# Kernel optimization log

Measured on AMD Instinct MI355X. Metric: run time of the kernel, lower is better.

Reference implementation:

```python
import jax, jax.numpy as jnp
import numpy as np

NUM_EXPERTS = 64
TOP_K = 8
NUM_TOKENS = 8192
HIDDEN = 1024
INTER = 512


def setup_inputs() -> dict:
    key = jax.random.key(0)
    k1, k2, k3, k4 = jax.random.split(key, 4)
    # 0.02 scale keeps activations in a sane range (randn weights with fan-in 1024)
    return {
        "hidden_states": jax.random.normal(k1, (NUM_TOKENS, HIDDEN), jnp.float32),
        "router_weight": jax.random.normal(k2, (HIDDEN, NUM_EXPERTS), jnp.float32) * 0.02,
        "merged_gate_up_proj": jax.random.normal(k3, (NUM_EXPERTS, HIDDEN, 2 * INTER), jnp.float32) * 0.02,
        "merged_down_proj": jax.random.normal(k4, (NUM_EXPERTS, INTER, HIDDEN), jnp.float32) * 0.02,
    }


def reference(hidden_states, router_weight, merged_gate_up_proj, merged_down_proj):
    T, H = hidden_states.shape
    E = router_weight.shape[1]

    # ---- Router: softmax over experts, top-k, renormalize top-k weights ----
    logits = hidden_states @ router_weight                       # [T, E]
    probs = jax.nn.softmax(logits, axis=-1)
    routing_weights, routing_indices = jax.lax.top_k(probs, TOP_K)  # [T, k]
    routing_weights = routing_weights / routing_weights.sum(-1, keepdims=True)

    # ---- Permute (haojun_permute_topk): replicate tokens topk times, stable-sort by expert ----
    flat_indices = routing_indices.reshape(-1)                   # [T*k]
    sort_order = jnp.argsort(flat_indices)                       # stable sort
    flat_states = jnp.repeat(hidden_states, TOP_K, axis=0)       # [T*k, H]
    permuted = flat_states[sort_order]                           # tokens grouped by expert
    group_sizes = jnp.bincount(flat_indices, length=E).astype(jnp.int32)  # tokens per expert

    # ---- Grouped MLP (grouped_gemm.gmm equivalent): y_i = x_i @ W[expert(i)] ----
    merged = jax.lax.ragged_dot(permuted, merged_gate_up_proj, group_sizes)  # [T*k, 2*I]
    gate, up = jnp.split(merged, 2, axis=-1)
    h = jax.nn.silu(gate) * up                                   # SiLU-gated (hidden_act='silu')
    expert_out = jax.lax.ragged_dot(h, merged_down_proj, group_sizes)        # [T*k, H]

    # ---- Unpermute: invert the sort, weight by routing probs, sum over top-k ----
    inv = jnp.argsort(sort_order)                                # unsort_order
    unpermuted = expert_out[inv].reshape(T, TOP_K, H)
    return (unpermuted * routing_weights[..., None]).sum(axis=1)  # [T, H]
```

## Files before the change

### kernel.cpp

```cpp
#include <hip/hip_runtime.h>
#include <cstdint>
#include <cstddef>

typedef __bf16 bf16_t;
typedef __bf16 bf16x8 __attribute__((ext_vector_type(8)));
typedef __bf16 bf16x4 __attribute__((ext_vector_type(4)));
typedef float f32x4 __attribute__((ext_vector_type(4)));

#define T_TOKENS 8192
#define HID 1024
#define INTER 512
#define NEXP 64
#define TOPK 8
#define NROWS (T_TOKENS * TOPK)
#define RT_TOK 16
#define NRBLK (T_TOKENS / RT_TOK)

typedef const unsigned int __attribute__((address_space(1)))* gptr_t;
typedef unsigned int __attribute__((address_space(3)))* lptr_t;

__device__ __forceinline__ void gload_lds16(const void* g, void* l) {
  __builtin_amdgcn_global_load_lds((gptr_t)g, (lptr_t)l, 16, 0, 0);
}

__device__ __forceinline__ f32x4 mfma16(bf16x8 a, bf16x8 b, f32x4 c) {
  return __builtin_amdgcn_mfma_f32_16x16x32_bf16(a, b, c, 0, 0, 0);
}

__device__ __forceinline__ int xcd_swizzle(int bid, int nwg) {
  int q = nwg >> 3;
  int xcd = bid & 7, i = bid >> 3;
  return xcd * q + i;
}

__global__ void transpose_cvt2_kernel(const float* __restrict__ w1, bf16_t* __restrict__ Wt1,
                                      const float* __restrict__ w2, bf16_t* __restrict__ Wt2,
                                      int* __restrict__ cntz) {
  const int tid = threadIdx.x;
  if (blockIdx.x == 0 && blockIdx.y == 0 && blockIdx.z == 0 && tid < 64) cntz[tid] = 0;

  const int e = blockIdx.z;
  const float* W; bf16_t* Wt; int K, k0;
  if (blockIdx.y < 16) {
    W = w1; Wt = Wt1; K = 1024; k0 = blockIdx.y * 64;
  } else {
    W = w2; Wt = Wt2; K = 512; k0 = (blockIdx.y - 16) * 64;
  }
  const int N = 1024;
  const int n0 = blockIdx.x * 64;

  __shared__ bf16_t tile[64][65];
  {
    const int r = tid >> 2, cq = tid & 3;
    const float* src = W + ((size_t)e * K + k0 + r) * N + n0 + cq * 16;
#pragma unroll
    for (int q = 0; q < 4; ++q) {
      float4 v = *(const float4*)(src + q * 4);
      tile[r][cq * 16 + q * 4 + 0] = (bf16_t)v.x;
      tile[r][cq * 16 + q * 4 + 1] = (bf16_t)v.y;
      tile[r][cq * 16 + q * 4 + 2] = (bf16_t)v.z;
      tile[r][cq * 16 + q * 4 + 3] = (bf16_t)v.w;
    }
  }
  __syncthreads();
  {
    const int nl = tid >> 2, kq = tid & 3;
    __align__(16) bf16_t tmp[16];
#pragma unroll
    for (int i = 0; i < 16; ++i) tmp[i] = tile[kq * 16 + i][nl];
    bf16_t* dst = Wt + ((size_t)e * N + n0 + nl) * K + k0 + kq * 16;
    *(bf16x8*)(dst + 0) = *(const bf16x8*)(tmp + 0);
    *(bf16x8*)(dst + 8) = *(const bf16x8*)(tmp + 8);
  }
}

__launch_bounds__(256, 2)
__global__ void router_kernel(const float* __restrict__ hs, const float* __restrict__ rw,
                              float* __restrict__ wval, int* __restrict__ widx,
                              bf16_t* __restrict__ hb, int* __restrict__ bcnt) {
  const int t0 = blockIdx.x * RT_TOK;
  const int tid = threadIdx.x;
  const int lane = tid & 63, w = tid >> 6;
  __shared__ float hsl[RT_TOK][HID / 4][4];
  __shared__ float part[4][RT_TOK][NEXP];
  int* bh = (int*)&hsl[0][0][0];

  for (int i = tid; i < RT_TOK * (HID / 4); i += 256) {
    int t = i >> 8, c = i & 255;
    float4 v = ((const float4*)(hs + (size_t)(t0 + t) * HID))[c];
    *(float4*)&hsl[t][c][0] = v;
    bf16x4 o;
    o[0] = (bf16_t)v.x; o[1] = (bf16_t)v.y; o[2] = (bf16_t)v.z; o[3] = (bf16_t)v.w;
    *(bf16x4*)(hb + (size_t)(t0 + t) * HID + c * 4) = o;
  }
  __syncthreads();

  float acc[RT_TOK];
#pragma unroll
  for (int t = 0; t < RT_TOK; ++t) acc[t] = 0.f;
  const int kb = w * 256;
  for (int kc = 0; kc < 64; ++kc) {
    const int k = kb + kc * 4;
    float r0 = rw[(size_t)(k + 0) * NEXP + lane];
    float r1 = rw[(size_t)(k + 1) * NEXP + lane];
    float r2 = rw[(size_t)(k + 2) * NEXP + lane];
    float r3 = rw[(size_t)(k + 3) * NEXP + lane];
#pragma unroll
    for (int t = 0; t < RT_TOK; ++t) {
      float4 hv = *(const float4*)&hsl[t][(kb >> 2) + kc][0];
      acc[t] = fmaf(hv.x, r0, acc[t]);
      acc[t] = fmaf(hv.y, r1, acc[t]);
      acc[t] = fmaf(hv.z, r2, acc[t]);
      acc[t] = fmaf(hv.w, r3, acc[t]);
    }
  }
#pragma unroll
  for (int t = 0; t < RT_TOK; ++t) part[w][t][lane] = acc[t];
  if (tid < NEXP) bh[tid] = 0;
  __syncthreads();

  for (int j = 0; j < 4; ++j) {
    const int t = w * 4 + j;
    float logit = part[0][t][lane] + part[1][t][lane] + part[2][t][lane] + part[3][t][lane];
    float m = logit;
    for (int off = 32; off; off >>= 1) m = fmaxf(m, __shfl_xor(m, off));
    float ex = expf(logit - m);
    float Z = ex;
    for (int off = 32; off; off >>= 1) Z += __shfl_xor(Z, off);
    float p = ex / Z;
    float sum8 = 0.f;
    float outv[8]; int outi[8];
#pragma unroll
    for (int s = 0; s < 8; ++s) {
      float v = p; int idx = lane;
      for (int off = 32; off; off >>= 1) {
        float vv = __shfl_xor(v, off);
        int ii = __shfl_xor(idx, off);
        if (vv > v || (vv == v && ii < idx)) { v = vv; idx = ii; }
      }
      outv[s] = v; outi[s] = idx; sum8 += v;
      if (lane == idx) p = -1.f;
    }
    if (lane == 0) {
      float inv = 1.f / sum8;
#pragma unroll
      for (int s = 0; s < 8; ++s) {
        wval[(size_t)(t0 + t) * TOPK + s] = outv[s] * inv;
        widx[(size_t)(t0 + t) * TOPK + s] = outi[s];
        atomicAdd(&bh[outi[s]], 1);
      }
    }
  }
  __syncthreads();
  if (tid < NEXP) bcnt[tid * NRBLK + blockIdx.x] = bh[tid];
}

__global__ void assign_kernel(const int* __restrict__ widx, const int* __restrict__ bcnt,
                              int* __restrict__ cnt2, int* __restrict__ row_org,
                              int* __restrict__ seg) {
  __shared__ int tot[NEXP];
  __shared__ int segl[NEXP];
  const int tid = threadIdx.x;
  if (tid < NEXP) {
    const int4* src = (const int4*)(bcnt + (size_t)tid * NRBLK);
    int a = 0;
    for (int j = 0; j < NRBLK / 4; ++j) { int4 v = src[j]; a += v.x + v.y + v.z + v.w; }
    tot[tid] = a;
  }
  __syncthreads();
  if (tid < NEXP) {
    int a = 0;
    for (int j = 0; j < tid; ++j) a += tot[j];
    segl[tid] = a;
    if (blockIdx.x == 0) {
      seg[tid] = a;
      if (tid == NEXP - 1) seg[NEXP] = a + tot[NEXP - 1];
    }
  }
  __syncthreads();
  for (int i = blockIdx.x * blockDim.x + tid; i < NROWS; i += gridDim.x * blockDim.x) {
    int e = widx[i];
    int p = segl[e] + atomicAdd(&cnt2[e], 1);
    row_org[p] = i;
  }
}

__launch_bounds__(256, 2)
__global__ void gemm1_kernel(const bf16_t* __restrict__ hb, const bf16_t* __restrict__ Wt1,
                             const int* __restrict__ row_org, const int* __restrict__ seg,
                             bf16_t* __restrict__ h) {
  const int bid = blockIdx.x + gridDim.x * (blockIdx.y + gridDim.y * blockIdx.z);
  const int swz = xcd_swizzle(bid, 16 * 4 * NEXP);
  const int mt = swz & 15;
  const int nt = (swz >> 4) & 3;
  const int e = swz >> 6;

  const int ms = seg[e];
  const int sz = seg[e + 1] - ms;
  const int n0 = nt * 128;
  const int tid = threadIdx.x;
  const int lane = tid & 63;
  const int wid = tid >> 6;
  const int wm = wid >> 1, wn = wid & 1;
  __shared__ __align__(16) bf16_t As[128 * 64];
  __shared__ __align__(16) bf16_t Bs[256 * 64];

  const int srow = tid >> 3;
  const int cg = (tid & 7) ^ (srow & 7);

  size_t boff[8];
#pragma unroll
  for (int b = 0; b < 8; ++b) {
    int brow = b * 32 + srow;
    int n = (brow < 128) ? (n0 + brow) : (512 + n0 + (brow - 128));
    boff[b] = ((size_t)e * 1024 + n) * 1024 + cg * 8;
  }
  const int l15 = lane & 15, l4 = lane >> 4;

  for (int m0 = mt * 128; m0 < sz; m0 += 16 * 128) {
    size_t aoff[4];
#pragma unroll
    for (int a = 0; a < 4; ++a) {
      int row = a * 32 + srow;
      int idx = m0 + row; if (idx >= sz) idx = sz - 1;
      aoff[a] = (size_t)(row_org[ms + idx] >> 3) * HID + cg * 8;
    }
    f32x4 accg[4][4], accu[4][4];
#pragma unroll
    for (int mi = 0; mi < 4; ++mi)
#pragma unroll
      for (int ni = 0; ni < 4; ++ni) {
        accg[mi][ni] = (f32x4){0.f, 0.f, 0.f, 0.f};
        accu[mi][ni] = (f32x4){0.f, 0.f, 0.f, 0.f};
      }

    for (int kt = 0; kt < 16; ++kt) {
      const int ko = kt * 64;
      __syncthreads();
#pragma unroll
      for (int a = 0; a < 4; ++a)
        gload_lds16(hb + aoff[a] + ko, (char*)As + a * 4096 + tid * 16);
#pragma unroll
      for (int b = 0; b < 8; ++b)
        gload_lds16(Wt1 + boff[b] + ko, (char*)Bs + b * 4096 + tid * 16);
      __syncthreads();
#pragma unroll
      for (int kf = 0; kf < 2; ++kf) {
        const int ch = kf * 4 + l4;
        bf16x8 af[4], bg[4], bu[4];
#pragma unroll
        for (int mi = 0; mi < 4; ++mi) {
          int r = wm * 64 + mi * 16 + l15;
          af[mi] = *(const bf16x8*)((const char*)As + r * 128 + ((ch ^ (r & 7)) << 4));
        }
#pragma unroll
        for (int ni = 0; ni < 4; ++ni) {
          int rg = wn * 64 + ni * 16 + l15;
          bg[ni] = *(const bf16x8*)((const char*)Bs + rg * 128 + ((ch ^ (rg & 7)) << 4));
          int ru = rg + 128;
          bu[ni] = *(const bf16x8*)((const char*)Bs + ru * 128 + ((ch ^ (ru & 7)) << 4));
        }
#pragma unroll
        for (int mi = 0; mi < 4; ++mi)
#pragma unroll
          for (int ni = 0; ni < 4; ++ni) {
            accg[mi][ni] = mfma16(af[mi], bg[ni], accg[mi][ni]);
            accu[mi][ni] = mfma16(af[mi], bu[ni], accu[mi][ni]);
          }
      }
    }
#pragma unroll
    for (int mi = 0; mi < 4; ++mi) {
#pragma unroll
      for (int j = 0; j < 4; ++j) {
        int mrow = wm * 64 + mi * 16 + l4 * 4 + j;
        int idx = m0 + mrow;
        if (idx < sz) {
          bf16_t* hrow = h + (size_t)(ms + idx) * INTER + n0 + wn * 64 + l15;
#pragma unroll
          for (int ni = 0; ni < 4; ++ni) {
            float g = accg[mi][ni][j];
            float u = accu[mi][ni][j];
            float s = g / (1.f + __expf(-g));
            hrow[ni * 16] = (bf16_t)(s * u);
          }
        }
      }
    }
  }
}

__launch_bounds__(256, 2)
__global__ void gemm2_kernel(const bf16_t* __restrict__ h, const bf16_t* __restrict__ Wt2,
                             const int* __restrict__ row_org, const int* __restrict__ seg,
                             bf16_t* __restrict__ eo) {
  const int bid = blockIdx.x + gridDim.x * (blockIdx.y + gridDim.y * blockIdx.z);
  const int swz = xcd_swizzle(bid, 16 * 8 * NEXP);
  const int mt = swz & 15;
  const int nt = (swz >> 4) & 7;
  const int e = swz >> 7;

  const int ms = seg[e];
  const int sz = seg[e + 1] - ms;
  const int n0 = nt * 128;
  const int tid = threadIdx.x;
  const int lane = tid & 63;
  const int wid = tid >> 6;
  const int wm = wid >> 1, wn = wid & 1;
  __shared__ __align__(16) bf16_t As[128 * 64];
  __shared__ __align__(16) bf16_t Bs[128 * 64];
  const int srow = tid >> 3;
  const int cg = (tid & 7) ^ (srow & 7);
  size_t boff[4];
#pragma unroll
  for (int b = 0; b < 4; ++b) {
    int brow = b * 32 + srow;
    boff[b] = ((size_t)e * 1024 + n0 + brow) * INTER + cg * 8;
  }
  const int l15 = lane & 15, l4 = lane >> 4;

  for (int m0 = mt * 128; m0 < sz; m0 += 16 * 128) {
    size_t aoff[4];
#pragma unroll
    for (int a = 0; a < 4; ++a) {
      int row = a * 32 + srow;
      int idx = m0 + row; if (idx >= sz) idx = sz - 1;
      aoff[a] = (size_t)(ms + idx) * INTER + cg * 8;
    }
    f32x4 acc[4][4];
#pragma unroll
    for (int mi = 0; mi < 4; ++mi)
#pragma unroll
      for (int ni = 0; ni < 4; ++ni) acc[mi][ni] = (f32x4){0.f, 0.f, 0.f, 0.f};

    for (int kt = 0; kt < 8; ++kt) {
      const int ko = kt * 64;
      __syncthreads();
#pragma unroll
      for (int a = 0; a < 4; ++a)
        gload_lds16(h + aoff[a] + ko, (char*)As + a * 4096 + tid * 16);
#pragma unroll
      for (int b = 0; b < 4; ++b)
        gload_lds16(Wt2 + boff[b] + ko, (char*)Bs + b * 4096 + tid * 16);
      __syncthreads();
#pragma unroll
      for (int kf = 0; kf < 2; ++kf) {
        const int ch = kf * 4 + l4;
        bf16x8 af[4], bb[4];
#pragma unroll
        for (int mi = 0; mi < 4; ++mi) {
          int r = wm * 64 + mi * 16 + l15;
          af[mi] = *(const bf16x8*)((const char*)As + r * 128 + ((ch ^ (r & 7)) << 4));
        }
#pragma unroll
        for (int ni = 0; ni < 4; ++ni) {
          int r = wn * 64 + ni * 16 + l15;
          bb[ni] = *(const bf16x8*)((const char*)Bs + r * 128 + ((ch ^ (r & 7)) << 4));
        }
#pragma unroll
        for (int mi = 0; mi < 4; ++mi)
#pragma unroll
          for (int ni = 0; ni < 4; ++ni)
            acc[mi][ni] = mfma16(af[mi], bb[ni], acc[mi][ni]);
      }
    }
#pragma unroll
    for (int mi = 0; mi < 4; ++mi) {
#pragma unroll
      for (int j = 0; j < 4; ++j) {
        int mrow = wm * 64 + mi * 16 + l4 * 4 + j;
        int idx = m0 + mrow;
        if (idx < sz) {
          int org = row_org[ms + idx];
          bf16_t* orow = eo + (size_t)org * HID + n0 + wn * 64 + l15;
#pragma unroll
          for (int ni = 0; ni < 4; ++ni)
            orow[ni * 16] = (bf16_t)acc[mi][ni][j];
        }
      }
    }
  }
}

__global__ void unpermute_kernel(const bf16_t* __restrict__ eo, const float* __restrict__ wval,
                                 float* __restrict__ out) {
  const int t = blockIdx.x * 2 + (threadIdx.x >> 7);
  const int c0 = (threadIdx.x & 127) * 8;
  float w[8];
#pragma unroll
  for (int s = 0; s < 8; ++s) w[s] = wval[(size_t)t * 8 + s];
  float acc[8] = {0.f, 0.f, 0.f, 0.f, 0.f, 0.f, 0.f, 0.f};
#pragma unroll
  for (int s = 0; s < 8; ++s) {
    bf16x8 v = *(const bf16x8*)(eo + ((size_t)t * 8 + s) * HID + c0);
#pragma unroll
    for (int q = 0; q < 8; ++q) acc[q] = fmaf(w[s], (float)v[q], acc[q]);
  }
  *(float4*)(out + (size_t)t * HID + c0) = *(float4*)&acc[0];
  *(float4*)(out + (size_t)t * HID + c0 + 4) = *(float4*)&acc[4];
}

extern "C" void kernel_launch(void* const* d_in, const int* in_sizes, int n_in,
                              void* d_out, int out_size, void* d_ws, size_t ws_size,
                              hipStream_t stream) {
  (void)in_sizes; (void)n_in; (void)ws_size; (void)out_size;
  const float* hs = (const float*)d_in[0];
  const float* rw = (const float*)d_in[1];
  const float* w1 = (const float*)d_in[2];
  const float* w2 = (const float*)d_in[3];
  float* out = (float*)d_out;

  char* p = (char*)d_ws;
  size_t off = 0;
  auto carve = [&](size_t bytes) {
    void* r = p + off;
    off = (off + bytes + 255) & ~(size_t)255;
    return r;
  };
  bf16_t* Wt1  = (bf16_t*)carve((size_t)NEXP * 1024 * 1024 * 2);
  bf16_t* Wt2  = (bf16_t*)carve((size_t)NEXP * 1024 * 512 * 2);
  bf16_t* hb   = (bf16_t*)carve((size_t)T_TOKENS * HID * 2);
  bf16_t* hmid = (bf16_t*)carve((size_t)NROWS * INTER * 2);
  float* wval  = (float*)carve((size_t)NROWS * 4);
  int* widx    = (int*)carve((size_t)NROWS * 4);
  int* row_org = (int*)carve((size_t)NROWS * 4);
  int* bcnt    = (int*)carve((size_t)NEXP * NRBLK * 4);
  int* cnt2    = (int*)carve(256);
  int* seg     = (int*)carve(66 * 4);

  bf16_t* eo = Wt1;

  transpose_cvt2_kernel<<<dim3(16, 24, 64), 256, 0, stream>>>(w1, Wt1, w2, Wt2, cnt2);
  router_kernel<<<NRBLK, 256, 0, stream>>>(hs, rw, wval, widx, hb, bcnt);
  assign_kernel<<<128, 256, 0, stream>>>(widx, bcnt, cnt2, row_org, seg);
  gemm1_kernel<<<dim3(16, 4, NEXP), 256, 0, stream>>>(hb, Wt1, row_org, seg, hmid);
  gemm2_kernel<<<dim3(16, 8, NEXP), 256, 0, stream>>>(hmid, Wt2, row_org, seg, eo);
  unpermute_kernel<<<T_TOKENS / 2, 256, 0, stream>>>(eo, wval, out);
}
```

Before: 604.1 us.

## Double-buffer LDS tiles in down-projection GEMM to overlap loads with MFMA

The down-projection grouped GEMM now keeps two LDS buffers for the A and B tiles. It prefetches the next K-slice through global_load_lds while MFMAs run on the current one, replacing the two barriers per iteration with one waitcnt and barrier. It also raises wave priority around the MFMA block. LDS use doubles to 64KB per block, which may limit how many blocks fit per CU under launch_bounds(256,2).

```diff
diff --git a/kernel.cpp b/kernel.cpp
--- a/kernel.cpp
+++ b/kernel.cpp
@@ -307,8 +307,8 @@
   const int lane = tid & 63;
   const int wid = tid >> 6;
   const int wm = wid >> 1, wn = wid & 1;
-  __shared__ __align__(16) bf16_t As[128 * 64];
-  __shared__ __align__(16) bf16_t Bs[128 * 64];
+  __shared__ __align__(16) bf16_t As[2][128 * 64];
+  __shared__ __align__(16) bf16_t Bs[2][128 * 64];
   const int srow = tid >> 3;
   const int cg = (tid & 7) ^ (srow & 7);
   size_t boff[4];
@@ -333,16 +333,27 @@
 #pragma unroll
       for (int ni = 0; ni < 4; ++ni) acc[mi][ni] = (f32x4){0.f, 0.f, 0.f, 0.f};
 
+#pragma unroll
+    for (int a = 0; a < 4; ++a)
+      gload_lds16(h + aoff[a], (char*)&As[0][0] + a * 4096 + tid * 16);
+#pragma unroll
+    for (int b = 0; b < 4; ++b)
+      gload_lds16(Wt2 + boff[b], (char*)&Bs[0][0] + b * 4096 + tid * 16);
+    asm volatile("s_waitcnt vmcnt(0)\n\ts_barrier" ::: "memory");
+
+    int cur = 0;
     for (int kt = 0; kt < 8; ++kt) {
-      const int ko = kt * 64;
-      __syncthreads();
-#pragma unroll
-      for (int a = 0; a < 4; ++a)
-        gload_lds16(h + aoff[a] + ko, (char*)As + a * 4096 + tid * 16);
-#pragma unroll
-      for (int b = 0; b < 4; ++b)
-        gload_lds16(Wt2 + boff[b] + ko, (char*)Bs + b * 4096 + tid * 16);
-      __syncthreads();
+      if (kt < 7) {
+        const int ko = (kt + 1) * 64;
+#pragma unroll
+        for (int a = 0; a < 4; ++a)
+          gload_lds16(h + aoff[a] + ko, (char*)&As[cur ^ 1][0] + a * 4096 + tid * 16);
+#pragma unroll
+        for (int b = 0; b < 4; ++b)
+          gload_lds16(Wt2 + boff[b] + ko, (char*)&Bs[cur ^ 1][0] + b * 4096 + tid * 16);
+      }
+      const char* Ab = (const char*)&As[cur][0];
+      const char* Bb = (const char*)&Bs[cur][0];
 #pragma unroll
       for (int kf = 0; kf < 2; ++kf) {
         const int ch = kf * 4 + l4;
@@ -350,19 +361,23 @@
 #pragma unroll
         for (int mi = 0; mi < 4; ++mi) {
           int r = wm * 64 + mi * 16 + l15;
-          af[mi] = *(const bf16x8*)((const char*)As + r * 128 + ((ch ^ (r & 7)) << 4));
+          af[mi] = *(const bf16x8*)(Ab + r * 128 + ((ch ^ (r & 7)) << 4));
         }
 #pragma unroll
         for (int ni = 0; ni < 4; ++ni) {
           int r = wn * 64 + ni * 16 + l15;
-          bb[ni] = *(const bf16x8*)((const char*)Bs + r * 128 + ((ch ^ (r & 7)) << 4));
-        }
+          bb[ni] = *(const bf16x8*)(Bb + r * 128 + ((ch ^ (r & 7)) << 4));
+        }
+        __builtin_amdgcn_s_setprio(1);
 #pragma unroll
         for (int mi = 0; mi < 4; ++mi)
 #pragma unroll
           for (int ni = 0; ni < 4; ++ni)
             acc[mi][ni] = mfma16(af[mi], bb[ni], acc[mi][ni]);
-      }
+        __builtin_amdgcn_s_setprio(0);
+      }
+      asm volatile("s_waitcnt vmcnt(0)\n\ts_barrier" ::: "memory");
+      cur ^= 1;
     }
 #pragma unroll
     for (int mi = 0; mi < 4; ++mi) {
```

Result: slower. 652.8 us (+8.1%).
